# Kernel optimization log

Measured on AMD Instinct MI355X. Metric: run time of the kernel, lower is better.

## Reference

```python
import jax, jax.numpy as jnp
import numpy as np

B, N, C, H = 32, 4096, 768, 12
D = C // H  # head dim
SCALE = D ** -0.5


def setup_inputs() -> dict:
    key = jax.random.key(0)
    ks = jax.random.split(key, 5)
    s = C ** -0.5
    return {
        "x": jax.random.normal(ks[0], (B, N, C), dtype=jnp.float32),
        "Wq": jax.random.normal(ks[1], (C, C), dtype=jnp.float32) * s,
        "Wkv": jax.random.normal(ks[2], (C, 2 * C), dtype=jnp.float32) * s,
        "Wp": jax.random.normal(ks[3], (C, C), dtype=jnp.float32) * s,
        "bp": jax.random.normal(ks[4], (C,), dtype=jnp.float32) * 0.01,
    }


def reference(x, Wq, Wkv, Wp, bp):
    b, n, c = x.shape
    h, d = H, c // H
    # single CLS query: [B,1,C] -> [B,H,1,d], pre-scaled
    q = (x[:, :1, :] @ Wq).reshape(b, 1, h, d).transpose(0, 2, 1, 3) * SCALE
    kv = (x @ Wkv).reshape(b, n, 2, h, d).transpose(2, 0, 3, 1, 4)
    k, v = kv[0], kv[1]
    # scores [B,H,1,N] -> softmax over N -> weighted V sum [B,H,1,d]
    attn = jax.nn.softmax(jnp.einsum("bhqd,bhnd->bhqn", q, k), axis=-1)
    cls = jnp.einsum("bhqn,bhnd->bhqd", attn, v).transpose(0, 2, 1, 3).reshape(b, 1, c)
    return cls @ Wp + bp
```

## Files before the change

kernel.cpp:

```cpp
#include <hip/hip_runtime.h>
#include <hip/hip_bf16.h>

#define B 32
#define N 4096
#define C 768
#define H 12
#define D 64
#define SCALE 0.125f

typedef __attribute__((ext_vector_type(4))) float f4;

__global__ void k_q(const float* __restrict__ x, const float* __restrict__ Wq,
                    float* __restrict__ q){
  int b = blockIdx.x; int tid = threadIdx.x;
  __shared__ float xs[C];
  for (int j = tid; j < C; j += 256) xs[j] = x[(size_t)b*N*C + j];
  __syncthreads();
  float a0=0.f, a1=0.f, a2=0.f;
  for (int c = 0; c < C; ++c){
    float xv = xs[c];
    const float* w = Wq + (size_t)c*C;
    a0 += xv*w[tid];
    a1 += xv*w[tid+256];
    a2 += xv*w[tid+512];
  }
  q[(size_t)b*C + tid]       = a0;
  q[(size_t)b*C + tid + 256] = a1;
  q[(size_t)b*C + tid + 512] = a2;
}

__global__ void k_r(const float* __restrict__ q, const float* __restrict__ Wkv,
                    float* __restrict__ r){
  int b = blockIdx.x, h = blockIdx.y, tid = threadIdx.x;
  __shared__ float qs[D];
  if (tid < D) qs[tid] = q[(size_t)b*C + h*D + tid] * SCALE;
  __syncthreads();
  for (int c = tid; c < C; c += 256){
    const float* w = Wkv + (size_t)c*(2*C) + h*D;
    float acc = 0.f;
    #pragma unroll 8
    for (int d = 0; d < D; ++d) acc += qs[d]*w[d];
    r[((size_t)b*H + h)*C + c] = acc;
  }
}

__global__ void k_scores(const float* __restrict__ x, const float* __restrict__ r,
                         float* __restrict__ spad){
  int b = blockIdx.x;
  int n = blockIdx.y*256 + threadIdx.x;
  const float* xp = x + ((size_t)b*N + n)*C;
  const float* rp = r + (size_t)b*H*C;
  float acc[H];
  #pragma unroll
  for (int h=0;h<H;h++) acc[h]=0.f;
  for (int c = 0; c < C; c += 4){
    f4 xv = *(const f4*)(xp + c);
    #pragma unroll
    for (int h=0;h<H;h++){
      const float* rr = rp + (size_t)h*C + c;
      acc[h] += xv[0]*rr[0] + xv[1]*rr[1] + xv[2]*rr[2] + xv[3]*rr[3];
    }
  }
  float* sp = spad + ((size_t)b*N + n)*16;
  #pragma unroll
  for (int h=0;h<H;h++) sp[h] = acc[h];
}

__global__ void k_softmax(float* __restrict__ spad){
  int b = blockIdx.x, tid = threadIdx.x;
  int g = tid >> 4, h = tid & 15;
  float* base = spad + (size_t)b*N*16;
  float m = -1e30f;
  for (int i = 0; i < 256; ++i) m = fmaxf(m, base[tid + 256*i]);
  __shared__ float red[16][17];
  red[g][h] = m; __syncthreads();
  for (int st = 8; st > 0; st >>= 1){
    if (g < st) red[g][h] = fmaxf(red[g][h], red[g+st][h]);
    __syncthreads();
  }
  m = red[0][h];
  __syncthreads();
  float l = 0.f;
  for (int i = 0; i < 256; ++i) l += __expf(base[tid + 256*i] - m);
  red[g][h] = l; __syncthreads();
  for (int st = 8; st > 0; st >>= 1){
    if (g < st) red[g][h] += red[g+st][h];
    __syncthreads();
  }
  float inv = 1.0f / red[0][h];
  for (int i = 0; i < 256; ++i){
    int idx = tid + 256*i;
    base[idx] = __expf(base[idx] - m) * inv;
  }
}

__global__ void k_xbar(const float* __restrict__ x, const float* __restrict__ spad,
                       float* __restrict__ xbar2){
  int b = blockIdx.x, slice = blockIdx.y, half = blockIdx.z;
  int tid = threadIdx.x, w = tid >> 6, lane = tid & 63;
  int c = slice*64 + lane;
  const float* xp = x + (size_t)b*N*C + c;
  const float* wp = spad + (size_t)b*N*16;
  float acc[H];
  #pragma unroll
  for (int h=0;h<H;h++) acc[h]=0.f;
  int n0 = half*2048 + w*512;
  for (int n = n0; n < n0+512; ++n){
    float xv = xp[(size_t)n*C];
    const float* ww = wp + (size_t)n*16;
    #pragma unroll
    for (int h=0;h<H;h++) acc[h] += ww[h]*xv;
  }
  __shared__ float red[4][H][64];
  #pragma unroll
  for (int h=0;h<H;h++) red[w][h][lane] = acc[h];
  __syncthreads();
  for (int o = tid; o < H*64; o += 256){
    int h = o >> 6, c2 = o & 63;
    float s = red[0][h][c2]+red[1][h][c2]+red[2][h][c2]+red[3][h][c2];
    xbar2[(((size_t)half*B + b)*H + h)*C + slice*64 + c2] = s;
  }
}

__global__ void k_cls(const float* __restrict__ xbar2, const float* __restrict__ Wkv,
                      float* __restrict__ cls){
  int b = blockIdx.x, h = blockIdx.y, tid = threadIdx.x;
  int d = tid & 63, part = tid >> 6;
  __shared__ float xs[C];
  for (int cc = tid; cc < C; cc += 256)
    xs[cc] = xbar2[((size_t)b*H + h)*C + cc] + xbar2[(((size_t)B + b)*H + h)*C + cc];
  __syncthreads();
  float acc = 0.f;
  int c0 = part*192;
  #pragma unroll 4
  for (int cc = c0; cc < c0+192; ++cc)
    acc += xs[cc] * Wkv[(size_t)cc*(2*C) + C + h*D + d];
  __shared__ float red[4][D];
  red[part][d] = acc; __syncthreads();
  if (tid < D)
    cls[(size_t)b*C + h*D + tid] = red[0][tid]+red[1][tid]+red[2][tid]+red[3][tid];
}

__global__ void k_out(const float* __restrict__ cls, const float* __restrict__ Wp,
                      const float* __restrict__ bp, float* __restrict__ out){
  int b = blockIdx.x, jb = blockIdx.y, tid = threadIdx.x;
  int j = jb*256 + tid;
  __shared__ float xs[C];
  for (int i = tid; i < C; i += 256) xs[i] = cls[(size_t)b*C + i];
  __syncthreads();
  float acc = bp[j];
  #pragma unroll 4
  for (int i = 0; i < C; ++i) acc += xs[i]*Wp[(size_t)i*C + j];
  out[(size_t)b*C + j] = acc;
}

extern "C" void kernel_launch(void* const* d_in, const int* in_sizes, int n_in,
                              void* d_out, int out_size, void* d_ws, size_t ws_size,
                              hipStream_t stream){
  const float* x   = (const float*)d_in[0];
  const float* Wq  = (const float*)d_in[1];
  const float* Wkv = (const float*)d_in[2];
  const float* Wp  = (const float*)d_in[3];
  const float* bp  = (const float*)d_in[4];
  float* out = (float*)d_out;
  char* ws = (char*)d_ws;
  float* q     = (float*)(ws + 0);
  float* r     = (float*)(ws + 98304);
  float* spad  = (float*)(ws + 1277952);
  float* xbar2 = (float*)(ws + 9666560);
  float* cls   = (float*)(ws + 12025856);

  k_q      <<<dim3(B),      dim3(256), 0, stream>>>(x, Wq, q);
  k_r      <<<dim3(B,H),    dim3(256), 0, stream>>>(q, Wkv, r);
  k_scores <<<dim3(B,16),   dim3(256), 0, stream>>>(x, r, spad);
  k_softmax<<<dim3(B),      dim3(256), 0, stream>>>(spad);
  k_xbar   <<<dim3(B,12,2), dim3(256), 0, stream>>>(x, spad, xbar2);
  k_cls    <<<dim3(B,H),    dim3(256), 0, stream>>>(xbar2, Wkv, cls);
  k_out    <<<dim3(B,3),    dim3(256), 0, stream>>>(cls, Wp, bp, out);
}
```

Baseline: 1.039 ms.

## Fuse scores, online softmax and weighted x-sum into one split-N kernel

Replaces the separate scores, softmax and xbar kernels with a single flash-decoding style kernel. Each block streams a 256-token chunk of x through LDS once, computes per-head scores, keeps an online softmax and accumulates the weighted x sums; k_cls then merges the partial results across 16 chunks. This reads x once instead of twice and drops the score scratch round-trips. It also splits k_q across more blocks and rewrites k_r with wave shuffles. The cost is heavy register use (36 accumulators plus cached r vectors), several barriers per 8-token tile, and only 512 blocks, which may limit occupancy.

```diff
diff --git a/kernel.cpp b/kernel.cpp
--- a/kernel.cpp
+++ b/kernel.cpp
@@ -1,5 +1,4 @@
 #include <hip/hip_runtime.h>
-#include <hip/hip_bf16.h>
 
 #define B 32
 #define N 4096
@@ -7,147 +6,234 @@
 #define H 12
 #define D 64
 #define SCALE 0.125f
+#define CH 16
+#define NT 256
+#define TILE 8
+#define NTILE 32
 
 typedef __attribute__((ext_vector_type(4))) float f4;
 
-__global__ void k_q(const float* __restrict__ x, const float* __restrict__ Wq,
-                    float* __restrict__ q){
-  int b = blockIdx.x; int tid = threadIdx.x;
+__global__ __launch_bounds__(256)
+void k_q(const float* __restrict__ x, const float* __restrict__ Wq,
+         float* __restrict__ q){
+  int b = blockIdx.x, jb = blockIdx.y, tid = threadIdx.x;
   __shared__ float xs[C];
-  for (int j = tid; j < C; j += 256) xs[j] = x[(size_t)b*N*C + j];
+  for (int c = tid; c < C; c += 256) xs[c] = x[(size_t)b*N*C + c];
   __syncthreads();
-  float a0=0.f, a1=0.f, a2=0.f;
-  for (int c = 0; c < C; ++c){
-    float xv = xs[c];
-    const float* w = Wq + (size_t)c*C;
-    a0 += xv*w[tid];
-    a1 += xv*w[tid+256];
-    a2 += xv*w[tid+512];
-  }
-  q[(size_t)b*C + tid]       = a0;
-  q[(size_t)b*C + tid + 256] = a1;
-  q[(size_t)b*C + tid + 512] = a2;
-}
-
-__global__ void k_r(const float* __restrict__ q, const float* __restrict__ Wkv,
-                    float* __restrict__ r){
+  int j = jb*256 + tid;
+  float acc = 0.f;
+  #pragma unroll 8
+  for (int c = 0; c < C; ++c) acc += xs[c] * Wq[(size_t)c*C + j];
+  q[(size_t)b*C + j] = acc;
+}
+
+__global__ __launch_bounds__(256)
+void k_r(const float* __restrict__ q, const float* __restrict__ Wkv,
+         float* __restrict__ r){
+  int b = blockIdx.x, h = blockIdx.y;
+  int tid = threadIdx.x, w = tid >> 6, lane = tid & 63;
+  float qv = q[(size_t)b*C + h*D + lane] * SCALE;
+  for (int c = w; c < C; c += 4){
+    float wv = Wkv[(size_t)c*(2*C) + h*D + lane];
+    float p = qv * wv;
+    #pragma unroll
+    for (int m = 1; m < 64; m <<= 1) p += __shfl_xor(p, m, 64);
+    if (lane == 0) r[((size_t)b*H + h)*C + c] = p;
+  }
+}
+
+__global__ __launch_bounds__(256)
+void k_fused(const float* __restrict__ x, const float* __restrict__ r,
+             float* __restrict__ pm, float* __restrict__ pl,
+             float* __restrict__ pxb){
+  int b = blockIdx.x, ch = blockIdx.y;
+  int tid = threadIdx.x, w = tid >> 6, lane = tid & 63;
+
+  __shared__ float xs[TILE][C];
+  __shared__ float scr[TILE][H][20];
+  __shared__ float sc[TILE][16];
+  __shared__ float wts[TILE][16];
+  __shared__ float als[16];
+
+  f4 rr4[3][3];
+  {
+    const float* rb = r + ((size_t)b*H + 3*w)*C + 4*lane;
+    #pragma unroll
+    for (int hh = 0; hh < 3; ++hh)
+      #pragma unroll
+      for (int jj = 0; jj < 3; ++jj)
+        rr4[hh][jj] = *(const f4*)(rb + hh*C + 256*jj);
+  }
+
+  float m0 = -1e30f, l0 = 0.f;
+  float xb[H][3];
+  #pragma unroll
+  for (int h = 0; h < H; ++h){ xb[h][0]=0.f; xb[h][1]=0.f; xb[h][2]=0.f; }
+
+  const float* gx = x + ((size_t)b*N + (size_t)ch*NT)*C;
+  f4 pf[6];
+  #pragma unroll
+  for (int k = 0; k < 6; ++k) pf[k] = ((const f4*)gx)[tid + 256*k];
+
+  for (int tt = 0; tt < NTILE; ++tt){
+    f4* xd = (f4*)&xs[0][0];
+    #pragma unroll
+    for (int k = 0; k < 6; ++k) xd[tid + 256*k] = pf[k];
+    if (tt + 1 < NTILE){
+      const f4* gn = (const f4*)(gx + (size_t)(tt+1)*TILE*C);
+      #pragma unroll
+      for (int k = 0; k < 6; ++k) pf[k] = gn[tid + 256*k];
+    }
+    __syncthreads();
+
+    float acc[TILE][3];
+    #pragma unroll
+    for (int t = 0; t < TILE; ++t){ acc[t][0]=0.f; acc[t][1]=0.f; acc[t][2]=0.f; }
+    #pragma unroll
+    for (int t = 0; t < TILE; ++t){
+      f4 p0 = *(const f4*)&xs[t][4*lane];
+      f4 p1 = *(const f4*)&xs[t][4*lane + 256];
+      f4 p2 = *(const f4*)&xs[t][4*lane + 512];
+      #pragma unroll
+      for (int hh = 0; hh < 3; ++hh){
+        f4 r0 = rr4[hh][0], r1 = rr4[hh][1], r2 = rr4[hh][2];
+        acc[t][hh] += p0.x*r0.x + p0.y*r0.y + p0.z*r0.z + p0.w*r0.w
+                    + p1.x*r1.x + p1.y*r1.y + p1.z*r1.z + p1.w*r1.w
+                    + p2.x*r2.x + p2.y*r2.y + p2.z*r2.z + p2.w*r2.w;
+      }
+    }
+    #pragma unroll
+    for (int t = 0; t < TILE; ++t)
+      #pragma unroll
+      for (int hh = 0; hh < 3; ++hh){
+        acc[t][hh] += __shfl_xor(acc[t][hh], 32, 64);
+        acc[t][hh] += __shfl_xor(acc[t][hh], 16, 64);
+      }
+    if (lane < 16){
+      #pragma unroll
+      for (int t = 0; t < TILE; ++t)
+        #pragma unroll
+        for (int hh = 0; hh < 3; ++hh)
+          scr[t][3*w + hh][lane] = acc[t][hh];
+    }
+    __syncthreads();
+
+    if (tid < 96){
+      int t8 = tid & 7, h12 = tid >> 3;
+      float s = 0.f;
+      #pragma unroll
+      for (int qq = 0; qq < 4; ++qq){
+        f4 v = *(const f4*)&scr[t8][h12][4*qq];
+        s += v.x + v.y + v.z + v.w;
+      }
+      sc[t8][h12] = s;
+    }
+    __syncthreads();
+
+    if (tid < H){
+      float tm = sc[0][tid];
+      #pragma unroll
+      for (int t = 1; t < TILE; ++t) tm = fmaxf(tm, sc[t][tid]);
+      float mnew = fmaxf(m0, tm);
+      float alpha = __expf(m0 - mnew);
+      float wsum = 0.f;
+      #pragma unroll
+      for (int t = 0; t < TILE; ++t){
+        float wv = __expf(sc[t][tid] - mnew);
+        wts[t][tid] = wv;
+        wsum += wv;
+      }
+      l0 = l0*alpha + wsum;
+      m0 = mnew;
+      als[tid] = alpha;
+    }
+    __syncthreads();
+
+    f4 av0 = *(const f4*)&als[0];
+    f4 av1 = *(const f4*)&als[4];
+    f4 av2 = *(const f4*)&als[8];
+    float alf[H] = {av0.x,av0.y,av0.z,av0.w, av1.x,av1.y,av1.z,av1.w,
+                    av2.x,av2.y,av2.z,av2.w};
+    #pragma unroll
+    for (int h = 0; h < H; ++h){
+      xb[h][0] *= alf[h]; xb[h][1] *= alf[h]; xb[h][2] *= alf[h];
+    }
+    #pragma unroll
+    for (int t = 0; t < TILE; ++t){
+      f4 w0 = *(const f4*)&wts[t][0];
+      f4 w1 = *(const f4*)&wts[t][4];
+      f4 w2 = *(const f4*)&wts[t][8];
+      float wf[H] = {w0.x,w0.y,w0.z,w0.w, w1.x,w1.y,w1.z,w1.w,
+                     w2.x,w2.y,w2.z,w2.w};
+      float x0 = xs[t][tid], x1 = xs[t][tid+256], x2 = xs[t][tid+512];
+      #pragma unroll
+      for (int h = 0; h < H; ++h){
+        xb[h][0] += wf[h]*x0;
+        xb[h][1] += wf[h]*x1;
+        xb[h][2] += wf[h]*x2;
+      }
+    }
+    __syncthreads();
+  }
+
+  size_t pbase = ((size_t)b*CH + ch)*H;
+  if (tid < H){ pm[pbase + tid] = m0; pl[pbase + tid] = l0; }
+  #pragma unroll
+  for (int h = 0; h < H; ++h){
+    size_t o = (pbase + h)*C + tid;
+    pxb[o]       = xb[h][0];
+    pxb[o + 256] = xb[h][1];
+    pxb[o + 512] = xb[h][2];
+  }
+}
+
+__global__ __launch_bounds__(256)
+void k_cls(const float* __restrict__ pm, const float* __restrict__ pl,
+           const float* __restrict__ pxb, const float* __restrict__ Wkv,
+           float* __restrict__ cls){
   int b = blockIdx.x, h = blockIdx.y, tid = threadIdx.x;
-  __shared__ float qs[D];
-  if (tid < D) qs[tid] = q[(size_t)b*C + h*D + tid] * SCALE;
+  __shared__ float xsm[C];
+  float M = -1e30f;
+  #pragma unroll
+  for (int c = 0; c < CH; ++c) M = fmaxf(M, pm[((size_t)b*CH + c)*H + h]);
+  float L = 0.f;
+  float eh[CH];
+  #pragma unroll
+  for (int c = 0; c < CH; ++c){
+    eh[c] = __expf(pm[((size_t)b*CH + c)*H + h] - M);
+    L += pl[((size_t)b*CH + c)*H + h]*eh[c];
+  }
+  float inv = 1.f/L;
+  #pragma unroll
+  for (int k = 0; k < 3; ++k){
+    int c = tid + 256*k;
+    float acc = 0.f;
+    #pragma unroll
+    for (int q = 0; q < CH; ++q)
+      acc += eh[q]*pxb[(((size_t)b*CH + q)*H + h)*C + c];
+    xsm[c] = acc*inv;
+  }
   __syncthreads();
-  for (int c = tid; c < C; c += 256){
-    const float* w = Wkv + (size_t)c*(2*C) + h*D;
-    float acc = 0.f;
-    #pragma unroll 8
-    for (int d = 0; d < D; ++d) acc += qs[d]*w[d];
-    r[((size_t)b*H + h)*C + c] = acc;
-  }
-}
-
-__global__ void k_scores(const float* __restrict__ x, const float* __restrict__ r,
-                         float* __restrict__ spad){
-  int b = blockIdx.x;
-  int n = blockIdx.y*256 + threadIdx.x;
-  const float* xp = x + ((size_t)b*N + n)*C;
-  const float* rp = r + (size_t)b*H*C;
-  float acc[H];
-  #pragma unroll
-  for (int h=0;h<H;h++) acc[h]=0.f;
-  for (int c = 0; c < C; c += 4){
-    f4 xv = *(const f4*)(xp + c);
-    #pragma unroll
-    for (int h=0;h<H;h++){
-      const float* rr = rp + (size_t)h*C + c;
-      acc[h] += xv[0]*rr[0] + xv[1]*rr[1] + xv[2]*rr[2] + xv[3]*rr[3];
-    }
-  }
-  float* sp = spad + ((size_t)b*N + n)*16;
-  #pragma unroll
-  for (int h=0;h<H;h++) sp[h] = acc[h];
-}
-
-__global__ void k_softmax(float* __restrict__ spad){
-  int b = blockIdx.x, tid = threadIdx.x;
-  int g = tid >> 4, h = tid & 15;
-  float* base = spad + (size_t)b*N*16;
-  float m = -1e30f;
-  for (int i = 0; i < 256; ++i) m = fmaxf(m, base[tid + 256*i]);
-  __shared__ float red[16][17];
-  red[g][h] = m; __syncthreads();
-  for (int st = 8; st > 0; st >>= 1){
-    if (g < st) red[g][h] = fmaxf(red[g][h], red[g+st][h]);
-    __syncthreads();
-  }
-  m = red[0][h];
-  __syncthreads();
-  float l = 0.f;
-  for (int i = 0; i < 256; ++i) l += __expf(base[tid + 256*i] - m);
-  red[g][h] = l; __syncthreads();
-  for (int st = 8; st > 0; st >>= 1){
-    if (g < st) red[g][h] += red[g+st][h];
-    __syncthreads();
-  }
-  float inv = 1.0f / red[0][h];
-  for (int i = 0; i < 256; ++i){
-    int idx = tid + 256*i;
-    base[idx] = __expf(base[idx] - m) * inv;
-  }
-}
-
-__global__ void k_xbar(const float* __restrict__ x, const float* __restrict__ spad,
-                       float* __restrict__ xbar2){
-  int b = blockIdx.x, slice = blockIdx.y, half = blockIdx.z;
-  int tid = threadIdx.x, w = tid >> 6, lane = tid & 63;
-  int c = slice*64 + lane;
-  const float* xp = x + (size_t)b*N*C + c;
-  const float* wp = spad + (size_t)b*N*16;
-  float acc[H];
-  #pragma unroll
-  for (int h=0;h<H;h++) acc[h]=0.f;
-  int n0 = half*2048 + w*512;
-  for (int n = n0; n < n0+512; ++n){
-    float xv = xp[(size_t)n*C];
-    const float* ww = wp + (size_t)n*16;
-    #pragma unroll
-    for (int h=0;h<H;h++) acc[h] += ww[h]*xv;
-  }
-  __shared__ float red[4][H][64];
-  #pragma unroll
-  for (int h=0;h<H;h++) red[w][h][lane] = acc[h];
-  __syncthreads();
-  for (int o = tid; o < H*64; o += 256){
-    int h = o >> 6, c2 = o & 63;
-    float s = red[0][h][c2]+red[1][h][c2]+red[2][h][c2]+red[3][h][c2];
-    xbar2[(((size_t)half*B + b)*H + h)*C + slice*64 + c2] = s;
-  }
-}
-
-__global__ void k_cls(const float* __restrict__ xbar2, const float* __restrict__ Wkv,
-                      float* __restrict__ cls){
-  int b = blockIdx.x, h = blockIdx.y, tid = threadIdx.x;
   int d = tid & 63, part = tid >> 6;
-  __shared__ float xs[C];
-  for (int cc = tid; cc < C; cc += 256)
-    xs[cc] = xbar2[((size_t)b*H + h)*C + cc] + xbar2[(((size_t)B + b)*H + h)*C + cc];
-  __syncthreads();
   float acc = 0.f;
   int c0 = part*192;
   #pragma unroll 4
-  for (int cc = c0; cc < c0+192; ++cc)
-    acc += xs[cc] * Wkv[(size_t)cc*(2*C) + C + h*D + d];
+  for (int cc = c0; cc < c0 + 192; ++cc)
+    acc += xsm[cc]*Wkv[(size_t)cc*(2*C) + C + h*D + d];
   __shared__ float red[4][D];
   red[part][d] = acc; __syncthreads();
   if (tid < D)
     cls[(size_t)b*C + h*D + tid] = red[0][tid]+red[1][tid]+red[2][tid]+red[3][tid];
 }
 
-__global__ void k_out(const float* __restrict__ cls, const float* __restrict__ Wp,
-                      const float* __restrict__ bp, float* __restrict__ out){
+__global__ __launch_bounds__(256)
+void k_out(const float* __restrict__ cls, const float* __restrict__ Wp,
+           const float* __restrict__ bp, float* __restrict__ out){
   int b = blockIdx.x, jb = blockIdx.y, tid = threadIdx.x;
-  int j = jb*256 + tid;
   __shared__ float xs[C];
   for (int i = tid; i < C; i += 256) xs[i] = cls[(size_t)b*C + i];
   __syncthreads();
+  int j = jb*256 + tid;
   float acc = bp[j];
   #pragma unroll 4
   for (int i = 0; i < C; ++i) acc += xs[i]*Wp[(size_t)i*C + j];
@@ -164,17 +250,16 @@
   const float* bp  = (const float*)d_in[4];
   float* out = (float*)d_out;
   char* ws = (char*)d_ws;
-  float* q     = (float*)(ws + 0);
-  float* r     = (float*)(ws + 98304);
-  float* spad  = (float*)(ws + 1277952);
-  float* xbar2 = (float*)(ws + 9666560);
-  float* cls   = (float*)(ws + 12025856);
-
-  k_q      <<<dim3(B),      dim3(256), 0, stream>>>(x, Wq, q);
-  k_r      <<<dim3(B,H),    dim3(256), 0, stream>>>(q, Wkv, r);
-  k_scores <<<dim3(B,16),   dim3(256), 0, stream>>>(x, r, spad);
-  k_softmax<<<dim3(B),      dim3(256), 0, stream>>>(spad);
-  k_xbar   <<<dim3(B,12,2), dim3(256), 0, stream>>>(x, spad, xbar2);
-  k_cls    <<<dim3(B,H),    dim3(256), 0, stream>>>(xbar2, Wkv, cls);
-  k_out    <<<dim3(B,3),    dim3(256), 0, stream>>>(cls, Wp, bp, out);
-}
+  float* q   = (float*)(ws + 0);
+  float* r   = (float*)(ws + 98304);
+  float* pm  = (float*)(ws + 1277952);
+  float* pl  = (float*)(ws + 1302528);
+  float* pxb = (float*)(ws + 1327104);
+  float* cls = (float*)(ws + 20201472);
+
+  k_q    <<<dim3(B,3),  dim3(256), 0, stream>>>(x, Wq, q);
+  k_r    <<<dim3(B,H),  dim3(256), 0, stream>>>(q, Wkv, r);
+  k_fused<<<dim3(B,CH), dim3(256), 0, stream>>>(x, r, pm, pl, pxb);
+  k_cls  <<<dim3(B,H),  dim3(256), 0, stream>>>(pm, pl, pxb, Wkv, cls);
+  k_out  <<<dim3(B,3),  dim3(256), 0, stream>>>(cls, Wp, bp, out);
+}
```

Result: faster. 882.4 us (-15.1%).
